# Performance work log

Hardware: AMD Instinct MI355X
Metric: run time of the kernel (lower is better)

Reference implementation:

```python
import jax, jax.numpy as jnp
import numpy as np

N = 4194304          # pixels (e.g. 2048x2048 render)
MOTION = 8
H = 8
OUT = 3
N_LAYERS = 3
Z_SCALE = 10.0
INV_SQRT_2PI = 1.0 / np.sqrt(2.0 * np.pi)

# activation set chosen from Fun.funs: sin, gaus, tanh, id
FUNS = [
    jnp.sin,
    lambda t: INV_SQRT_2PI * jnp.exp(-0.5 * t * t),  # 'gaus'
    jnp.tanh,
    lambda t: t,                                      # 'id'
]


def _make_masks(rng):
    # mirror __init__: per layer, permute H cells and split into len(Funs) sorted groups
    masks = []
    for _ in range(N_LAYERS):
        perm = rng.permutation(H)
        masks.append([np.sort(a) for a in np.array_split(perm, len(FUNS))])
    return jnp.asarray(np.array(masks), dtype=jnp.int64)  # [L, F, H/F]


def setup_inputs() -> dict:
    key = jax.random.key(0)
    ks = jax.random.split(key, 10)
    rng = np.random.default_rng(0)
    return {
        "x": jax.random.normal(ks[0], (N, 1), jnp.float32),
        "y": jax.random.normal(ks[1], (N, 1), jnp.float32),
        "r": jax.random.uniform(ks[2], (N, 1), jnp.float32),
        "z": jax.random.normal(ks[3], (N, MOTION), jnp.float32),
        "W0": jax.random.normal(ks[4], (H, MOTION + 3), jnp.float32) * 0.3,
        "b0": jax.random.normal(ks[5], (H,), jnp.float32) * 0.1,
        "Wm": jax.random.normal(ks[6], (H, H), jnp.float32) * 0.3,
        "bm": jax.random.normal(ks[7], (H,), jnp.float32) * 0.1,
        "Wo": jax.random.normal(ks[8], (OUT, H), jnp.float32) * 0.3,
        "bo": jax.random.normal(ks[9], (OUT,), jnp.float32) * 0.1,
        "masks": _make_masks(rng),
    }


def reference(x, y, r, z, W0, b0, Wm, bm, Wo, bo, masks):
    inp = jnp.concatenate([z / Z_SCALE, x, y, r], axis=1)  # [N, MOTION+3]
    out = inp @ W0.T + b0                                  # [N, H]
    for l in range(N_LAYERS):
        # NOTE: original repeats the same Linear module -> shared Wm/bm across layers
        pre = out @ Wm.T + bm
        new_out = jnp.zeros_like(out)
        for f, fn in enumerate(FUNS):
            m = masks[l, f]                                # disjoint column group
            new_out = new_out.at[:, m].set(fn(pre[:, m]))
        out = (new_out + out) * 0.5
    return jax.nn.sigmoid(out @ Wo.T + bo)                 # [N, OUT]
```

## Files before the change

kernel.cpp:

```cpp
#include <hip/hip_runtime.h>


__global__ void cppn_prep(const float* __restrict__ W0,
                          const float* __restrict__ b0,
                          const float* __restrict__ Wm,
                          const float* __restrict__ bm,
                          const float* __restrict__ Wo,
                          const float* __restrict__ bo,
                          const int* __restrict__ masks,
                          float* __restrict__ wf,
                          int* __restrict__ wi) {
    int t = threadIdx.x;
    if (t < 88) {
        int k = t % 11;
        wf[t] = W0[t] * (k < 8 ? 0.1f : 1.0f);
    } else if (t < 96) {
        wf[t] = b0[t - 88];
    } else if (t < 288) {
        int j = t - 96;
        int l = j >> 6;
        float s = (l == 0) ? 1.0f : (l == 1 ? 0.5f : 0.25f);
        wf[96 + j] = Wm[j & 63] * s;
    } else if (t < 296) {
        wf[t] = bm[t - 288];
    } else if (t < 320) {
        wf[t] = Wo[t - 296] * 0.125f;
    } else if (t < 323) {
        wf[t] = bo[t - 320];
    } else if (t < 323 + 24) {
        int j = t - 323;
        bool is64 = true;
        for (int q = 1; q < 24; q += 2) is64 = is64 && (masks[q] == 0);
        int c = is64 ? masks[2 * j] : masks[j];
        int l = j >> 3;
        int f = (j & 7) >> 1;
        wi[384 + l * 8 + c] = f;
    }
}

#define PX 2

__global__ __launch_bounds__(256) void cppn_main(
    const float* __restrict__ xb,
    const float* __restrict__ yb,
    const float* __restrict__ rb,
    const float4* __restrict__ zb,
    const float* __restrict__ wf,
    const int* __restrict__ fid,
    float* __restrict__ out,
    int n) {
    int base = blockIdx.x * (256 * PX) + threadIdx.x;
    int idx[PX];
    bool ok[PX];
#pragma unroll
    for (int px = 0; px < PX; ++px) {
        idx[px] = base + px * 256;
        ok[px] = idx[px] < n;
    }

    float in[PX][11];
#pragma unroll
    for (int px = 0; px < PX; ++px) {
        int i = ok[px] ? idx[px] : 0;
        float4 z0 = zb[2 * i];
        float4 z1 = zb[2 * i + 1];
        in[px][0] = z0.x; in[px][1] = z0.y; in[px][2] = z0.z; in[px][3] = z0.w;
        in[px][4] = z1.x; in[px][5] = z1.y; in[px][6] = z1.z; in[px][7] = z1.w;
        in[px][8]  = xb[i];
        in[px][9]  = yb[i];
        in[px][10] = rb[i];
    }

    float u[PX][8];
#pragma unroll
    for (int h = 0; h < 8; ++h) {
#pragma unroll
        for (int px = 0; px < PX; ++px) {
            float acc = wf[88 + h];
#pragma unroll
            for (int k = 0; k < 11; ++k)
                acc = fmaf(wf[h * 11 + k], in[px][k], acc);
            u[px][h] = acc;
        }
    }

#pragma unroll
    for (int l = 0; l < 3; ++l) {
        const float* W = wf + 96 + 64 * l;
        const float scale = (l == 0) ? 1.0f : (l == 1 ? 2.0f : 4.0f);
        float p[PX][8];
#pragma unroll
        for (int h = 0; h < 8; ++h) {
#pragma unroll
            for (int px = 0; px < PX; ++px) {
                float acc = wf[288 + h];
#pragma unroll
                for (int k = 0; k < 8; ++k)
                    acc = fmaf(W[h * 8 + k], u[px][k], acc);
                p[px][h] = acc;
            }
        }
#pragma unroll
        for (int h = 0; h < 8; ++h) {
            int f = __builtin_amdgcn_readfirstlane(fid[l * 8 + h]);
            float v[PX];
            if (f == 0) {
#pragma unroll
                for (int px = 0; px < PX; ++px) v[px] = __sinf(p[px][h]);
            } else if (f == 1) {
#pragma unroll
                for (int px = 0; px < PX; ++px) {
                    float t = p[px][h];
                    v[px] = 0.3989422804014327f * __expf(-0.5f * t * t);
                }
            } else if (f == 2) {
#pragma unroll
                for (int px = 0; px < PX; ++px) {
                    float e = __expf(2.0f * p[px][h]);
                    v[px] = fmaf(-2.0f, __builtin_amdgcn_rcpf(e + 1.0f), 1.0f);
                }
            } else {
#pragma unroll
                for (int px = 0; px < PX; ++px) v[px] = p[px][h];
            }
#pragma unroll
            for (int px = 0; px < PX; ++px)
                u[px][h] = fmaf(scale, v[px], u[px][h]);
        }
    }

#pragma unroll
    for (int j = 0; j < 3; ++j) {
#pragma unroll
        for (int px = 0; px < PX; ++px) {
            float acc = wf[320 + j];
#pragma unroll
            for (int k = 0; k < 8; ++k)
                acc = fmaf(wf[296 + j * 8 + k], u[px][k], acc);
            float e = __expf(-acc);
            float v = __builtin_amdgcn_rcpf(1.0f + e);
            if (ok[px]) out[3 * idx[px] + j] = v;
        }
    }
}

extern "C" void kernel_launch(void* const* d_in, const int* in_sizes, int n_in,
                              void* d_out, int out_size, void* d_ws, size_t ws_size,
                              hipStream_t stream) {
    const float* xb = (const float*)d_in[0];
    const float* yb = (const float*)d_in[1];
    const float* rb = (const float*)d_in[2];
    const float* zb = (const float*)d_in[3];
    const float* W0 = (const float*)d_in[4];
    const float* b0 = (const float*)d_in[5];
    const float* Wm = (const float*)d_in[6];
    const float* bm = (const float*)d_in[7];
    const float* Wo = (const float*)d_in[8];
    const float* bo = (const float*)d_in[9];
    const int* masks = (const int*)d_in[10];

    float* wf = (float*)d_ws;
    int*   wi = (int*)d_ws;

    int n = in_sizes[0];

    cppn_prep<<<1, 512, 0, stream>>>(W0, b0, Wm, bm, Wo, bo, masks, wf, wi);
    int per_block = 256 * PX;
    cppn_main<<<(n + per_block - 1) / per_block, 256, 0, stream>>>(
        xb, yb, rb, (const float4*)zb, wf, wi + 384,
        (float*)d_out, n);
}
```

Baseline: 258.1 us.

## Convert main kernel to grid-stride loop with register prefetch of next tile

The main kernel now launches at most 1024 blocks that loop over the pixel range in grid strides instead of one block per tile. Inside the loop, the inputs for the next tile are loaded into registers while the current tile's MLP layers are computed, so memory latency can overlap with ALU work. This raises register pressure, which may lower occupancy, and 1024 blocks may underfill the GPU relative to latency-hiding needs.

```diff
diff --git a/kernel.cpp b/kernel.cpp
--- a/kernel.cpp
+++ b/kernel.cpp
@@ -39,6 +39,28 @@
 }
 
 #define PX 2
+#define TPB 256
+#define TILE (TPB * PX)
+
+__device__ __forceinline__ void load_tile(const float* __restrict__ xb,
+                                          const float* __restrict__ yb,
+                                          const float* __restrict__ rb,
+                                          const float4* __restrict__ zb,
+                                          int base, int n,
+                                          float (&in)[PX][11]) {
+#pragma unroll
+    for (int px = 0; px < PX; ++px) {
+        int i = base + px * TPB;
+        if (i >= n) i = 0;
+        float4 z0 = zb[2 * i];
+        float4 z1 = zb[2 * i + 1];
+        in[px][0] = z0.x; in[px][1] = z0.y; in[px][2] = z0.z; in[px][3] = z0.w;
+        in[px][4] = z1.x; in[px][5] = z1.y; in[px][6] = z1.z; in[px][7] = z1.w;
+        in[px][8]  = xb[i];
+        in[px][9]  = yb[i];
+        in[px][10] = rb[i];
+    }
+}
 
 __global__ __launch_bounds__(256) void cppn_main(
     const float* __restrict__ xb,
@@ -48,99 +70,97 @@
     const float* __restrict__ wf,
     const int* __restrict__ fid,
     float* __restrict__ out,
-    int n) {
-    int base = blockIdx.x * (256 * PX) + threadIdx.x;
-    int idx[PX];
-    bool ok[PX];
-#pragma unroll
-    for (int px = 0; px < PX; ++px) {
-        idx[px] = base + px * 256;
-        ok[px] = idx[px] < n;
-    }
+    int n, int sweep) {
+    int tid = threadIdx.x;
+    int base = blockIdx.x * TILE + tid;
 
-    float in[PX][11];
-#pragma unroll
-    for (int px = 0; px < PX; ++px) {
-        int i = ok[px] ? idx[px] : 0;
-        float4 z0 = zb[2 * i];
-        float4 z1 = zb[2 * i + 1];
-        in[px][0] = z0.x; in[px][1] = z0.y; in[px][2] = z0.z; in[px][3] = z0.w;
-        in[px][4] = z1.x; in[px][5] = z1.y; in[px][6] = z1.z; in[px][7] = z1.w;
-        in[px][8]  = xb[i];
-        in[px][9]  = yb[i];
-        in[px][10] = rb[i];
-    }
+    float cur[PX][11];
+    if (base < n) load_tile(xb, yb, rb, zb, base, n, cur);
 
-    float u[PX][8];
-#pragma unroll
-    for (int h = 0; h < 8; ++h) {
-#pragma unroll
-        for (int px = 0; px < PX; ++px) {
-            float acc = wf[88 + h];
-#pragma unroll
-            for (int k = 0; k < 11; ++k)
-                acc = fmaf(wf[h * 11 + k], in[px][k], acc);
-            u[px][h] = acc;
-        }
-    }
+    for (; base < n; base += sweep) {
+        int nbase = base + sweep;
 
-#pragma unroll
-    for (int l = 0; l < 3; ++l) {
-        const float* W = wf + 96 + 64 * l;
-        const float scale = (l == 0) ? 1.0f : (l == 1 ? 2.0f : 4.0f);
-        float p[PX][8];
+        float u[PX][8];
 #pragma unroll
         for (int h = 0; h < 8; ++h) {
 #pragma unroll
             for (int px = 0; px < PX; ++px) {
-                float acc = wf[288 + h];
+                float acc = wf[88 + h];
+#pragma unroll
+                for (int k = 0; k < 11; ++k)
+                    acc = fmaf(wf[h * 11 + k], cur[px][k], acc);
+                u[px][h] = acc;
+            }
+        }
+
+        float nxt[PX][11];
+        if (nbase < n) load_tile(xb, yb, rb, zb, nbase, n, nxt);
+
+#pragma unroll
+        for (int l = 0; l < 3; ++l) {
+            const float* W = wf + 96 + 64 * l;
+            const float scale = (l == 0) ? 1.0f : (l == 1 ? 2.0f : 4.0f);
+            float p[PX][8];
+#pragma unroll
+            for (int h = 0; h < 8; ++h) {
+#pragma unroll
+                for (int px = 0; px < PX; ++px) {
+                    float acc = wf[288 + h];
+#pragma unroll
+                    for (int k = 0; k < 8; ++k)
+                        acc = fmaf(W[h * 8 + k], u[px][k], acc);
+                    p[px][h] = acc;
+                }
+            }
+#pragma unroll
+            for (int h = 0; h < 8; ++h) {
+                int f = __builtin_amdgcn_readfirstlane(fid[l * 8 + h]);
+                float v[PX];
+                if (f == 0) {
+#pragma unroll
+                    for (int px = 0; px < PX; ++px) v[px] = __sinf(p[px][h]);
+                } else if (f == 1) {
+#pragma unroll
+                    for (int px = 0; px < PX; ++px) {
+                        float t = p[px][h];
+                        v[px] = 0.3989422804014327f * __expf(-0.5f * t * t);
+                    }
+                } else if (f == 2) {
+#pragma unroll
+                    for (int px = 0; px < PX; ++px) {
+                        float e = __expf(2.0f * p[px][h]);
+                        v[px] = fmaf(-2.0f, __builtin_amdgcn_rcpf(e + 1.0f), 1.0f);
+                    }
+                } else {
+#pragma unroll
+                    for (int px = 0; px < PX; ++px) v[px] = p[px][h];
+                }
+#pragma unroll
+                for (int px = 0; px < PX; ++px)
+                    u[px][h] = fmaf(scale, v[px], u[px][h]);
+            }
+        }
+
+#pragma unroll
+        for (int j = 0; j < 3; ++j) {
+#pragma unroll
+            for (int px = 0; px < PX; ++px) {
+                float acc = wf[320 + j];
 #pragma unroll
                 for (int k = 0; k < 8; ++k)
-                    acc = fmaf(W[h * 8 + k], u[px][k], acc);
-                p[px][h] = acc;
+                    acc = fmaf(wf[296 + j * 8 + k], u[px][k], acc);
+                float e = __expf(-acc);
+                float v = __builtin_amdgcn_rcpf(1.0f + e);
+                int i = base + px * TPB;
+                if (i < n) out[3 * i + j] = v;
             }
         }
-#pragma unroll
-        for (int h = 0; h < 8; ++h) {
-            int f = __builtin_amdgcn_readfirstlane(fid[l * 8 + h]);
-            float v[PX];
-            if (f == 0) {
-#pragma unroll
-                for (int px = 0; px < PX; ++px) v[px] = __sinf(p[px][h]);
-            } else if (f == 1) {
-#pragma unroll
-                for (int px = 0; px < PX; ++px) {
-                    float t = p[px][h];
-                    v[px] = 0.3989422804014327f * __expf(-0.5f * t * t);
-                }
-            } else if (f == 2) {
-#pragma unroll
-                for (int px = 0; px < PX; ++px) {
-                    float e = __expf(2.0f * p[px][h]);
-                    v[px] = fmaf(-2.0f, __builtin_amdgcn_rcpf(e + 1.0f), 1.0f);
-                }
-            } else {
-#pragma unroll
-                for (int px = 0; px < PX; ++px) v[px] = p[px][h];
-            }
-#pragma unroll
-            for (int px = 0; px < PX; ++px)
-                u[px][h] = fmaf(scale, v[px], u[px][h]);
-        }
-    }
 
 #pragma unroll
-    for (int j = 0; j < 3; ++j) {
+        for (int px = 0; px < PX; ++px)
 #pragma unroll
-        for (int px = 0; px < PX; ++px) {
-            float acc = wf[320 + j];
-#pragma unroll
-            for (int k = 0; k < 8; ++k)
-                acc = fmaf(wf[296 + j * 8 + k], u[px][k], acc);
-            float e = __expf(-acc);
-            float v = __builtin_amdgcn_rcpf(1.0f + e);
-            if (ok[px]) out[3 * idx[px] + j] = v;
-        }
+            for (int k = 0; k < 11; ++k)
+                cur[px][k] = nxt[px][k];
     }
 }
 
@@ -165,8 +185,11 @@
     int n = in_sizes[0];
 
     cppn_prep<<<1, 512, 0, stream>>>(W0, b0, Wm, bm, Wo, bo, masks, wf, wi);
-    int per_block = 256 * PX;
-    cppn_main<<<(n + per_block - 1) / per_block, 256, 0, stream>>>(
+
+    int nb = (n + TILE - 1) / TILE;
+    int blocks = nb < 1024 ? nb : 1024;
+    int sweep = blocks * TILE;
+    cppn_main<<<blocks, 256, 0, stream>>>(
         xb, yb, rb, (const float4*)zb, wf, wi + 384,
-        (float*)d_out, n);
+        (float*)d_out, n, sweep);
 }
```

Result: slower. 328.1 us (+27.1%).
